# Optimization experiments

Hardware: AMD Instinct MI355X
Metric: run time of the kernel (lower is better)

Reference implementation:

```python
import jax, jax.numpy as jnp
import numpy as np

N_NODES = 50000
N_EDGES = 800000
HIDDEN = 128
NUM_LAYERS = 3
NEG_SLOPE = 0.2  # PyG GATConv default leaky_relu slope


def setup_inputs() -> dict:
    key = jax.random.key(0)
    ks = jax.random.split(key, 10)
    d = HIDDEN
    glorot = 1.0 / np.sqrt(d)
    inp = {
        "x": jax.random.normal(ks[0], (N_NODES, d), dtype=jnp.float32),
        "edge_index": jax.random.randint(ks[1], (2, N_EDGES), 0, N_NODES, dtype=jnp.int32),
        "edge_mask": jax.random.uniform(ks[2], (N_EDGES,), dtype=jnp.float32),
        # GATConv params (heads=1)
        "W_gat": jax.random.normal(ks[3], (d, d), dtype=jnp.float32) * glorot,
        "a_src": jax.random.normal(ks[4], (d,), dtype=jnp.float32) * glorot,
        "a_dst": jax.random.normal(ks[5], (d,), dtype=jnp.float32) * glorot,
        "b_gat": jnp.zeros((d,), dtype=jnp.float32),
        # Stacked GCNConv params
        "W_gcn": jax.random.normal(ks[6], (NUM_LAYERS, d, d), dtype=jnp.float32) * glorot,
        "b_gcn": jnp.zeros((NUM_LAYERS, d), dtype=jnp.float32),
    }
    return inp


def _seg_softmax(e, seg, n):
    m = jax.ops.segment_max(e, seg, num_segments=n)
    p = jnp.exp(e - m[seg])
    s = jax.ops.segment_sum(p, seg, num_segments=n)
    return p / s[seg]


def reference(x, edge_index, edge_mask, W_gat, a_src, a_dst, b_gat, W_gcn, b_gcn):
    N = x.shape[0]
    loops = jnp.arange(N, dtype=edge_index.dtype)
    src = jnp.concatenate([edge_index[0], loops])  # [E+N] with self loops
    dst = jnp.concatenate([edge_index[1], loops])

    # --- GATConv (heads=1, add_self_loops=True); edge_attr ignored (edge_dim=None) ---
    xp = x @ W_gat                                      # [N, d]
    e = jax.nn.leaky_relu((xp @ a_src)[src] + (xp @ a_dst)[dst], NEG_SLOPE)
    alpha = _seg_softmax(e, dst, N)                     # segment softmax over incoming edges
    h = jax.ops.segment_sum(alpha[:, None] * xp[src], dst, num_segments=N) + b_gat

    # --- GCN normalization with edge_mask as edge_weight (self-loop weight = 1) ---
    w = jnp.concatenate([edge_mask, jnp.ones((N,), dtype=edge_mask.dtype)])
    deg = jax.ops.segment_sum(w, dst, num_segments=N)
    dinv = jnp.where(deg > 0, jax.lax.rsqrt(jnp.maximum(deg, 1e-12)), 0.0)
    norm = dinv[src] * w * dinv[dst]                    # [E+N]

    outs = [h]
    for l in range(NUM_LAYERS):
        z = outs[-1] @ W_gcn[l]                         # [N, d]
        z = jax.ops.segment_sum(norm[:, None] * z[src], dst, num_segments=N) + b_gcn[l]
        outs.append(jax.nn.relu(z))

    # JumpingKnowledge 'max': elementwise max over layer outputs
    return jnp.max(jnp.stack(outs, axis=0), axis=0)
```

## Files before the change

### kernel.cpp

```cpp
#include <hip/hip_runtime.h>

#define HIDDEN 128
#define NEG_SLOPE 0.2f
#define P_SORT 256

typedef unsigned short ushort_t;
typedef __attribute__((ext_vector_type(8))) short short8;
typedef __attribute__((ext_vector_type(4))) float floatx4;

static inline size_t align_up(size_t x, size_t a){ return (x + a - 1) & ~(a - 1); }

__device__ __forceinline__ ushort_t f2b(float f){
  unsigned u = __float_as_uint(f);
  unsigned r = (u + 0x7FFFu + ((u >> 16) & 1u)) >> 16;
  return (ushort_t)r;
}

__device__ __forceinline__ void fma8(float* acc, uint4 v, float a){
  acc[0] += a * __uint_as_float(v.x << 16);
  acc[1] += a * __uint_as_float(v.x & 0xFFFF0000u);
  acc[2] += a * __uint_as_float(v.y << 16);
  acc[3] += a * __uint_as_float(v.y & 0xFFFF0000u);
  acc[4] += a * __uint_as_float(v.z << 16);
  acc[5] += a * __uint_as_float(v.z & 0xFFFF0000u);
  acc[6] += a * __uint_as_float(v.w << 16);
  acc[7] += a * __uint_as_float(v.w & 0xFFFF0000u);
}

__device__ __forceinline__ uint4 pack8(const float* f){
  uint4 u;
  u.x = (unsigned)f2b(f[0]) | ((unsigned)f2b(f[1]) << 16);
  u.y = (unsigned)f2b(f[2]) | ((unsigned)f2b(f[3]) << 16);
  u.z = (unsigned)f2b(f[4]) | ((unsigned)f2b(f[5]) << 16);
  u.w = (unsigned)f2b(f[6]) | ((unsigned)f2b(f[7]) << 16);
  return u;
}


__global__ __launch_bounds__(256) void k_b1cnt(const int* __restrict__ dst,
                                               int* __restrict__ bcnt,
                                               int E, int epb, int nbkt){
  __shared__ unsigned c[256];
  int t = threadIdx.x;
  c[t] = 0;
  __syncthreads();
  int e0 = blockIdx.x * epb;
  int e1 = min(E, e0 + epb);
  for (int e = e0 + t; e < e1; e += 256) atomicAdd(&c[dst[e] >> 8], 1u);
  __syncthreads();
  if (t < nbkt) bcnt[t * P_SORT + blockIdx.x] = (int)c[t];
}

__global__ void k_scan1(const int* __restrict__ in, int* __restrict__ incl,
                        int* __restrict__ blockSums, int M){
  __shared__ int sd[256];
  int t = threadIdx.x;
  int i = blockIdx.x*256 + t;
  int v = (i < M) ? in[i] : 0;
  sd[t] = v; __syncthreads();
  for (int off = 1; off < 256; off <<= 1){
    int add = (t >= off) ? sd[t-off] : 0;
    __syncthreads();
    sd[t] += add;
    __syncthreads();
  }
  if (i < M) incl[i] = sd[t];
  if (t == 255) blockSums[blockIdx.x] = sd[255];
}

__global__ void k_scan2(const int* __restrict__ blockSums, int* __restrict__ blockOffs, int nb){
  __shared__ int sd[256];
  __shared__ int carry;
  int t = threadIdx.x;
  if (t == 0) carry = 0;
  __syncthreads();
  for (int base = 0; base < nb; base += 256){
    int i = base + t;
    int v = (i < nb) ? blockSums[i] : 0;
    sd[t] = v; __syncthreads();
    for (int off = 1; off < 256; off <<= 1){
      int add = (t >= off) ? sd[t-off] : 0;
      __syncthreads();
      sd[t] += add;
      __syncthreads();
    }
    if (i < nb) blockOffs[i] = carry + sd[t] - v;
    __syncthreads();
    if (t == 0) carry += sd[255];
    __syncthreads();
  }
}

__global__ void k_scanex(int* __restrict__ arr, const int* __restrict__ in,
                         const int* __restrict__ blockOffs, int M){
  int i = blockIdx.x*256 + threadIdx.x;
  if (i < M) arr[i] = arr[i] - in[i] + blockOffs[blockIdx.x];
}

__global__ __launch_bounds__(256) void k_b1place(const int* __restrict__ src,
                                                 const int* __restrict__ dst,
                                                 const float* __restrict__ w,
                                                 const int* __restrict__ ebase,
                                                 unsigned* __restrict__ tpk,
                                                 float* __restrict__ tw,
                                                 int E, int epb){
  __shared__ unsigned c[256];
  int t = threadIdx.x;
  c[t] = 0;
  __syncthreads();
  int e0 = blockIdx.x * epb;
  int e1 = min(E, e0 + epb);
  for (int e = e0 + t; e < e1; e += 256){
    int d = dst[e];
    int b = d >> 8;
    unsigned r = atomicAdd(&c[b], 1u);
    int pos = ebase[b * P_SORT + blockIdx.x] + (int)r;
    tpk[pos] = (unsigned)src[e] | ((unsigned)(d & 255) << 16);
    tw[pos]  = w[e];
  }
}

__global__ __launch_bounds__(256) void k_b2(const unsigned* __restrict__ tpk,
                                            const float* __restrict__ tw,
                                            const int* __restrict__ ebase,
                                            int* __restrict__ col_src,
                                            float* __restrict__ col_w,
                                            int* __restrict__ rowp,
                                            float* __restrict__ dinv,
                                            int N, int E, int nbkt){
  __shared__ unsigned hcnt[256];
  __shared__ int sd[256];
  __shared__ int lofs[256];
  __shared__ unsigned rcnt[256];
  __shared__ float wsum[256];
  int b = blockIdx.x, t = threadIdx.x;
  int e0 = ebase[b * P_SORT];
  int e1 = (b + 1 < nbkt) ? ebase[(b + 1) * P_SORT] : E;
  hcnt[t] = 0; rcnt[t] = 0; wsum[t] = 0.f;
  __syncthreads();
  for (int e = e0 + t; e < e1; e += 256) atomicAdd(&hcnt[(tpk[e] >> 16) & 255u], 1u);
  __syncthreads();
  int v = (int)hcnt[t];
  sd[t] = v; __syncthreads();
  for (int off = 1; off < 256; off <<= 1){
    int add = (t >= off) ? sd[t-off] : 0;
    __syncthreads();
    sd[t] += add;
    __syncthreads();
  }
  lofs[t] = sd[t] - v;
  int node = b*256 + t;
  if (node < N) rowp[node] = e0 + sd[t] - v;
  if (b == 0 && t == 0) rowp[N] = E;
  __syncthreads();
  for (int e = e0 + t; e < e1; e += 256){
    unsigned pk = tpk[e];
    float wv = tw[e];
    unsigned dl = (pk >> 16) & 255u;
    unsigned r = atomicAdd(&rcnt[dl], 1u);
    int pos = e0 + lofs[dl] + (int)r;
    col_src[pos] = (int)(pk & 0xFFFFu);
    col_w[pos]   = wv;
    atomicAdd(&wsum[dl], wv);
  }
  __syncthreads();
  if (node < N) dinv[node] = rsqrtf(wsum[t] + 1.0f);
}

__global__ void k_edges(const int* __restrict__ rowp, const int* __restrict__ col_src,
                        const float* __restrict__ col_w, const float* __restrict__ dinv,
                        const float* __restrict__ ssrc, const float* __restrict__ sdst,
                        float* __restrict__ col_norm, float* __restrict__ col_e, int N){
  int n = blockIdx.x*16 + (threadIdx.x >> 4);
  int l = threadIdx.x & 15;
  if (n >= N) return;
  int rs = rowp[n], re = rowp[n+1];
  float dn = dinv[n], sd = sdst[n];
  for (int j = rs + l; j < re; j += 16){
    int s = col_src[j];
    col_norm[j] = dinv[s] * col_w[j] * dn;
    float ee = ssrc[s] + sd;
    col_e[j] = (ee >= 0.f) ? ee : NEG_SLOPE*ee;
  }
}


__global__ void k_cast_x(const float* __restrict__ x, unsigned* __restrict__ xb, long n2){
  long i = (long)blockIdx.x*256 + threadIdx.x;
  if (i >= n2) return;
  float2 v = ((const float2*)x)[i];
  xb[i] = (unsigned)f2b(v.x) | ((unsigned)f2b(v.y) << 16);
}

__global__ void k_cast_w(const float* __restrict__ Wg, const float* __restrict__ Wc,
                         ushort_t* __restrict__ Wt){
  int i = blockIdx.x*256 + threadIdx.x;
  int mat = i >> 14, idx = i & 16383;
  int k = idx >> 7, n = idx & 127;
  float v = (mat == 0) ? Wg[idx] : Wc[(mat-1)*16384 + idx];
  Wt[mat*16384 + n*128 + k] = f2b(v);
}

__global__ __launch_bounds__(256) void k_gemm(const ushort_t* __restrict__ A,
                                              const ushort_t* __restrict__ Wt,
                                              ushort_t* __restrict__ C, int M){
  int wave = threadIdx.x >> 6, l = threadIdx.x & 63;
  int q = l >> 4, lm = l & 15;
  int rowBase = blockIdx.x*128 + wave*32;
  floatx4 acc[2][8];
  #pragma unroll
  for (int mt = 0; mt < 2; mt++)
    #pragma unroll
    for (int nt = 0; nt < 8; nt++) acc[mt][nt] = (floatx4){0.f,0.f,0.f,0.f};

  #pragma unroll
  for (int kc = 0; kc < 4; kc++){
    int k0 = kc*32 + q*8;
    short8 a[2];
    #pragma unroll
    for (int mt = 0; mt < 2; mt++){
      long r = rowBase + mt*16 + lm;
      if (r < M) a[mt] = *(const short8*)(A + r*128 + k0);
      else       a[mt] = (short8){0,0,0,0,0,0,0,0};
    }
    #pragma unroll
    for (int nt = 0; nt < 8; nt++){
      short8 b = *(const short8*)(Wt + (nt*16 + lm)*128 + k0);
      acc[0][nt] = __builtin_amdgcn_mfma_f32_16x16x32_bf16(a[0], b, acc[0][nt], 0, 0, 0);
      acc[1][nt] = __builtin_amdgcn_mfma_f32_16x16x32_bf16(a[1], b, acc[1][nt], 0, 0, 0);
    }
  }
  #pragma unroll
  for (int mt = 0; mt < 2; mt++){
    #pragma unroll
    for (int r = 0; r < 4; r++){
      long row = rowBase + mt*16 + q*4 + r;
      if (row < M){
        #pragma unroll
        for (int nt = 0; nt < 8; nt++)
          C[row*128 + nt*16 + lm] = f2b(acc[mt][nt][r]);
      }
    }
  }
}

__global__ void k_sdots(const unsigned* __restrict__ xb, const float* __restrict__ a_src,
                        const float* __restrict__ a_dst, float* __restrict__ ssrc,
                        float* __restrict__ sdst, int N){
  int n = blockIdx.x*4 + (threadIdx.x >> 6);
  int lane = threadIdx.x & 63;
  if (n >= N) return;
  unsigned w = xb[(size_t)n*64 + lane];
  float v0 = __uint_as_float(w << 16);
  float v1 = __uint_as_float(w & 0xFFFF0000u);
  float2 as = ((const float2*)a_src)[lane];
  float2 ad = ((const float2*)a_dst)[lane];
  float ps = v0*as.x + v1*as.y;
  float pd = v0*ad.x + v1*ad.y;
  #pragma unroll
  for (int off = 32; off >= 1; off >>= 1){
    ps += __shfl_xor(ps, off, 64);
    pd += __shfl_xor(pd, off, 64);
  }
  if (lane == 0){ ssrc[n] = ps; sdst[n] = pd; }
}

__global__ void k_gat(const ushort_t* __restrict__ xb, const int* __restrict__ rowp,
                      const int* __restrict__ col_src, const float* __restrict__ col_e,
                      const float* __restrict__ ssrc, const float* __restrict__ sdst,
                      const float* __restrict__ b_gat, ushort_t* __restrict__ hb,
                      float* __restrict__ y, int N){
  int n = blockIdx.x*4 + (threadIdx.x >> 6);
  int l = threadIdx.x & 63;
  if (n >= N) return;
  int rs = rowp[n], re = rowp[n+1];
  float es = ssrc[n] + sdst[n];
  es = (es >= 0.f) ? es : NEG_SLOPE*es;
  float m = es;
  for (int j = rs + l; j < re; j += 64) m = fmaxf(m, col_e[j]);
  #pragma unroll
  for (int off = 32; off >= 1; off >>= 1) m = fmaxf(m, __shfl_xor(m, off, 64));
  float s = 0.f;
  for (int j = rs + l; j < re; j += 64) s += __expf(col_e[j] - m);
  #pragma unroll
  for (int off = 32; off >= 1; off >>= 1) s += __shfl_xor(s, off, 64);
  s += __expf(es - m);
  float inv = 1.f / s;
  float a0 = __expf(es - m) * inv;

  int sub = l >> 4, q = l & 15;
  const uint4* x16 = (const uint4*)xb;
  float acc[8] = {0.f,0.f,0.f,0.f,0.f,0.f,0.f,0.f};
  int deg = re - rs;
  int iters = (deg + 3) >> 2;
  for (int i = 0; i < iters; i++){
    int edge = rs + (i << 2) + sub;
    float a = 0.f; int sidx = n;
    if (edge < re){ sidx = col_src[edge]; a = __expf(col_e[edge] - m) * inv; }
    uint4 v = x16[(size_t)sidx*16 + q];
    fma8(acc, v, a);
  }
  #pragma unroll
  for (int j = 0; j < 8; j++){
    acc[j] += __shfl_xor(acc[j], 16, 64);
    acc[j] += __shfl_xor(acc[j], 32, 64);
  }
  if (sub == 0){
    uint4 v = x16[(size_t)n*16 + q];
    fma8(acc, v, a0);
    float4 b0 = ((const float4*)b_gat)[q*2];
    float4 b1 = ((const float4*)b_gat)[q*2 + 1];
    acc[0]+=b0.x; acc[1]+=b0.y; acc[2]+=b0.z; acc[3]+=b0.w;
    acc[4]+=b1.x; acc[5]+=b1.y; acc[6]+=b1.z; acc[7]+=b1.w;
    ((uint4*)hb)[(size_t)n*16 + q] = pack8(acc);
    float4* y4 = (float4*)y;
    y4[(size_t)n*32 + q*2]     = make_float4(acc[0], acc[1], acc[2], acc[3]);
    y4[(size_t)n*32 + q*2 + 1] = make_float4(acc[4], acc[5], acc[6], acc[7]);
  }
}

__global__ void k_gcn(const ushort_t* __restrict__ zb, const int* __restrict__ rowp,
                      const int* __restrict__ col_src, const float* __restrict__ col_norm,
                      const float* __restrict__ dinv, const float* __restrict__ bias,
                      ushort_t* __restrict__ hb, float* __restrict__ y, int N){
  int n = blockIdx.x*4 + (threadIdx.x >> 6);
  int l = threadIdx.x & 63;
  if (n >= N) return;
  int rs = rowp[n], re = rowp[n+1];
  float di = dinv[n];
  float sn = di * di;
  int sub = l >> 4, q = l & 15;
  const uint4* z16 = (const uint4*)zb;
  float acc[8] = {0.f,0.f,0.f,0.f,0.f,0.f,0.f,0.f};
  int deg = re - rs;
  int iters = (deg + 3) >> 2;
  for (int i = 0; i < iters; i++){
    int edge = rs + (i << 2) + sub;
    float a = 0.f; int sidx = n;
    if (edge < re){ sidx = col_src[edge]; a = col_norm[edge]; }
    uint4 v = z16[(size_t)sidx*16 + q];
    fma8(acc, v, a);
  }
  #pragma unroll
  for (int j = 0; j < 8; j++){
    acc[j] += __shfl_xor(acc[j], 16, 64);
    acc[j] += __shfl_xor(acc[j], 32, 64);
  }
  if (sub == 0){
    uint4 v = z16[(size_t)n*16 + q];
    fma8(acc, v, sn);
    float4 b0 = ((const float4*)bias)[q*2];
    float4 b1 = ((const float4*)bias)[q*2 + 1];
    acc[0]=fmaxf(acc[0]+b0.x,0.f); acc[1]=fmaxf(acc[1]+b0.y,0.f);
    acc[2]=fmaxf(acc[2]+b0.z,0.f); acc[3]=fmaxf(acc[3]+b0.w,0.f);
    acc[4]=fmaxf(acc[4]+b1.x,0.f); acc[5]=fmaxf(acc[5]+b1.y,0.f);
    acc[6]=fmaxf(acc[6]+b1.z,0.f); acc[7]=fmaxf(acc[7]+b1.w,0.f);
    ((uint4*)hb)[(size_t)n*16 + q] = pack8(acc);
    float4* y4 = (float4*)y;
    float4 y0 = y4[(size_t)n*32 + q*2];
    float4 y1 = y4[(size_t)n*32 + q*2 + 1];
    y0.x=fmaxf(y0.x,acc[0]); y0.y=fmaxf(y0.y,acc[1]); y0.z=fmaxf(y0.z,acc[2]); y0.w=fmaxf(y0.w,acc[3]);
    y1.x=fmaxf(y1.x,acc[4]); y1.y=fmaxf(y1.y,acc[5]); y1.z=fmaxf(y1.z,acc[6]); y1.w=fmaxf(y1.w,acc[7]);
    y4[(size_t)n*32 + q*2]     = y0;
    y4[(size_t)n*32 + q*2 + 1] = y1;
  }
}

extern "C" void kernel_launch(void* const* d_in, const int* in_sizes, int n_in,
                              void* d_out, int out_size, void* d_ws, size_t ws_size,
                              hipStream_t stream){
  const float* x      = (const float*)d_in[0];
  const int*   eidx   = (const int*)d_in[1];
  const float* emask  = (const float*)d_in[2];
  const float* W_gat  = (const float*)d_in[3];
  const float* a_src  = (const float*)d_in[4];
  const float* a_dst  = (const float*)d_in[5];
  const float* b_gat  = (const float*)d_in[6];
  const float* W_gcn  = (const float*)d_in[7];
  const float* b_gcn  = (const float*)d_in[8];
  int N = in_sizes[0] / HIDDEN;
  int E = in_sizes[1] / 2;
  const int* src = eidx;
  const int* dst = eidx + E;

  char* p = (char*)d_ws;
  auto carve = [&](size_t bytes)->char*{ char* q = p; p += align_up(bytes, 512); return q; };
  ushort_t* xb   = (ushort_t*)carve((size_t)N*HIDDEN*2);
  ushort_t* zb   = (ushort_t*)carve((size_t)N*HIDDEN*2);
  ushort_t* hb   = (ushort_t*)carve((size_t)N*HIDDEN*2);
  ushort_t* Wt   = (ushort_t*)carve((size_t)4*HIDDEN*HIDDEN*2);
  float* ssrc    = (float*)carve((size_t)N*4);
  float* sdst    = (float*)carve((size_t)N*4);
  float* dinv    = (float*)carve((size_t)N*4);
  int*   rowp    = (int*)  carve((size_t)(N+1)*4);
  int*   col_src = (int*)  carve((size_t)E*4);
  float* col_w   = (float*)carve((size_t)E*4);
  float* col_norm= (float*)carve((size_t)E*4);
  float* col_e   = (float*)carve((size_t)E*4);
  unsigned* tpk  = (unsigned*)carve((size_t)E*4);
  float* tw      = (float*)carve((size_t)E*4);
  int nbkt = (N + 255) >> 8;
  int M    = nbkt * P_SORT;
  int*   bcnt  = (int*)carve((size_t)M*4);
  int*   ebase = (int*)carve((size_t)M*4);
  int nbs = (M + 255) / 256;
  int*   blockSums = (int*)carve((size_t)nbs*4);
  int*   blockOffs = (int*)carve((size_t)nbs*4);
  (void)ws_size; (void)n_in; (void)out_size;

  int epb = (E + P_SORT - 1) / P_SORT;
  int gb  = (N + 127) / 128;
  int nwb = (N + 3) / 4;
  int nqb = (N + 15) / 16;
  long n2 = (long)N*64;
  int cb  = (int)((n2 + 255) / 256);

  k_b1cnt  <<<P_SORT, 256, 0, stream>>>(dst, bcnt, E, epb, nbkt);
  k_scan1  <<<nbs, 256, 0, stream>>>(bcnt, ebase, blockSums, M);
  k_scan2  <<<1,   256, 0, stream>>>(blockSums, blockOffs, nbs);
  k_scanex <<<nbs, 256, 0, stream>>>(ebase, bcnt, blockOffs, M);
  k_b1place<<<P_SORT, 256, 0, stream>>>(src, dst, emask, ebase, tpk, tw, E, epb);
  k_b2     <<<nbkt, 256, 0, stream>>>(tpk, tw, ebase, col_src, col_w, rowp, dinv, N, E, nbkt);

  k_cast_x<<<cb, 256, 0, stream>>>(x, (unsigned*)xb, n2);
  k_cast_w<<<(4*HIDDEN*HIDDEN)/256, 256, 0, stream>>>(W_gat, W_gcn, Wt);

  k_gemm <<<gb, 256, 0, stream>>>(xb, Wt, zb, N);
  k_sdots<<<nwb,256, 0, stream>>>((const unsigned*)zb, a_src, a_dst, ssrc, sdst, N);
  k_edges<<<nqb,256, 0, stream>>>(rowp, col_src, col_w, dinv, ssrc, sdst, col_norm, col_e, N);

  k_gat  <<<nwb,256, 0, stream>>>(zb, rowp, col_src, col_e, ssrc, sdst,
                                  b_gat, hb, (float*)d_out, N);
  for (int l = 0; l < 3; l++){
    k_gemm<<<gb, 256, 0, stream>>>(hb, Wt + (size_t)(l+1)*HIDDEN*HIDDEN, zb, N);
    k_gcn <<<nwb,256, 0, stream>>>(zb, rowp, col_src, col_norm, dinv,
                                   b_gcn + (size_t)l*HIDDEN, hb, (float*)d_out, N);
  }
}
```

Before: 393.9 us.

## Split feature aggregation into column chunks and precompute softmax coefficients

Softmax normalization moves into a separate k_soft kernel that writes per-edge alpha in place of col_e, plus a per-node self coefficient. GAT and GCN aggregation are merged into one templated k_agg that splits the 128 features into 4 column chunks, each handled by its own block group. Each wave now walks 16 edges at a time with 4 lanes per row chunk. This gives four times as many waves and more edges in flight per wave, aimed at hiding gather latency. The cost is that col_src and coefficients are re-read once per chunk and there is an extra launch plus a pass over col_e.

```diff
diff --git a/kernel.cpp b/kernel.cpp
--- a/kernel.cpp
+++ b/kernel.cpp
@@ -184,6 +184,29 @@
   }
 }
 
+__global__ void k_soft(const int* __restrict__ rowp, float* __restrict__ col_e,
+                       const float* __restrict__ ssrc, const float* __restrict__ sdst,
+                       float* __restrict__ selfa, int N){
+  int n = blockIdx.x*4 + (threadIdx.x >> 6);
+  int l = threadIdx.x & 63;
+  if (n >= N) return;
+  int rs = rowp[n], re = rowp[n+1];
+  float es = ssrc[n] + sdst[n];
+  es = (es >= 0.f) ? es : NEG_SLOPE*es;
+  float m = es;
+  for (int j = rs + l; j < re; j += 64) m = fmaxf(m, col_e[j]);
+  #pragma unroll
+  for (int off = 32; off >= 1; off >>= 1) m = fmaxf(m, __shfl_xor(m, off, 64));
+  float s = 0.f;
+  for (int j = rs + l; j < re; j += 64) s += __expf(col_e[j] - m);
+  #pragma unroll
+  for (int off = 32; off >= 1; off >>= 1) s += __shfl_xor(s, off, 64);
+  s += __expf(es - m);
+  float inv = 1.f / s;
+  for (int j = rs + l; j < re; j += 64) col_e[j] = __expf(col_e[j] - m) * inv;
+  if (l == 0) selfa[n] = __expf(es - m) * inv;
+}
+
 
 __global__ void k_cast_x(const float* __restrict__ x, unsigned* __restrict__ xb, long n2){
   long i = (long)blockIdx.x*256 + threadIdx.x;
@@ -265,104 +288,64 @@
   if (lane == 0){ ssrc[n] = ps; sdst[n] = pd; }
 }
 
-__global__ void k_gat(const ushort_t* __restrict__ xb, const int* __restrict__ rowp,
-                      const int* __restrict__ col_src, const float* __restrict__ col_e,
-                      const float* __restrict__ ssrc, const float* __restrict__ sdst,
-                      const float* __restrict__ b_gat, ushort_t* __restrict__ hb,
-                      float* __restrict__ y, int N){
-  int n = blockIdx.x*4 + (threadIdx.x >> 6);
+template<int MODE>
+__global__ __launch_bounds__(256) void k_agg(const ushort_t* __restrict__ feat,
+                                             const int* __restrict__ rowp,
+                                             const int* __restrict__ col_src,
+                                             const float* __restrict__ coef,
+                                             const float* __restrict__ selfc,
+                                             const float* __restrict__ bias,
+                                             ushort_t* __restrict__ out,
+                                             float* __restrict__ y, int N, int nwb){
+  int c   = blockIdx.x / nwb;
+  int blk = blockIdx.x - c*nwb;
+  int n = blk*4 + (threadIdx.x >> 6);
+  if (n >= N) return;
   int l = threadIdx.x & 63;
-  if (n >= N) return;
+  int sub = l >> 2, q = l & 3;
   int rs = rowp[n], re = rowp[n+1];
-  float es = ssrc[n] + sdst[n];
-  es = (es >= 0.f) ? es : NEG_SLOPE*es;
-  float m = es;
-  for (int j = rs + l; j < re; j += 64) m = fmaxf(m, col_e[j]);
-  #pragma unroll
-  for (int off = 32; off >= 1; off >>= 1) m = fmaxf(m, __shfl_xor(m, off, 64));
-  float s = 0.f;
-  for (int j = rs + l; j < re; j += 64) s += __expf(col_e[j] - m);
-  #pragma unroll
-  for (int off = 32; off >= 1; off >>= 1) s += __shfl_xor(s, off, 64);
-  s += __expf(es - m);
-  float inv = 1.f / s;
-  float a0 = __expf(es - m) * inv;
-
-  int sub = l >> 4, q = l & 15;
-  const uint4* x16 = (const uint4*)xb;
+  const uint4* f16 = (const uint4*)feat;
   float acc[8] = {0.f,0.f,0.f,0.f,0.f,0.f,0.f,0.f};
-  int deg = re - rs;
-  int iters = (deg + 3) >> 2;
-  for (int i = 0; i < iters; i++){
-    int edge = rs + (i << 2) + sub;
+  for (int base = rs; base < re; base += 16){
+    int edge = base + sub;
     float a = 0.f; int sidx = n;
-    if (edge < re){ sidx = col_src[edge]; a = __expf(col_e[edge] - m) * inv; }
-    uint4 v = x16[(size_t)sidx*16 + q];
+    if (edge < re){ sidx = col_src[edge]; a = coef[edge]; }
+    uint4 v = f16[(size_t)sidx*16 + c*4 + q];
     fma8(acc, v, a);
   }
   #pragma unroll
   for (int j = 0; j < 8; j++){
+    acc[j] += __shfl_xor(acc[j], 4, 64);
+    acc[j] += __shfl_xor(acc[j], 8, 64);
     acc[j] += __shfl_xor(acc[j], 16, 64);
     acc[j] += __shfl_xor(acc[j], 32, 64);
   }
   if (sub == 0){
-    uint4 v = x16[(size_t)n*16 + q];
-    fma8(acc, v, a0);
-    float4 b0 = ((const float4*)b_gat)[q*2];
-    float4 b1 = ((const float4*)b_gat)[q*2 + 1];
+    float sc = selfc[n];
+    if (MODE == 1) sc = sc * sc;
+    uint4 v = f16[(size_t)n*16 + c*4 + q];
+    fma8(acc, v, sc);
+    float4 b0 = ((const float4*)bias)[c*8 + q*2];
+    float4 b1 = ((const float4*)bias)[c*8 + q*2 + 1];
     acc[0]+=b0.x; acc[1]+=b0.y; acc[2]+=b0.z; acc[3]+=b0.w;
     acc[4]+=b1.x; acc[5]+=b1.y; acc[6]+=b1.z; acc[7]+=b1.w;
-    ((uint4*)hb)[(size_t)n*16 + q] = pack8(acc);
+    if (MODE == 1){
+      #pragma unroll
+      for (int j = 0; j < 8; j++) acc[j] = fmaxf(acc[j], 0.f);
+    }
+    ((uint4*)out)[(size_t)n*16 + c*4 + q] = pack8(acc);
     float4* y4 = (float4*)y;
-    y4[(size_t)n*32 + q*2]     = make_float4(acc[0], acc[1], acc[2], acc[3]);
-    y4[(size_t)n*32 + q*2 + 1] = make_float4(acc[4], acc[5], acc[6], acc[7]);
-  }
-}
-
-__global__ void k_gcn(const ushort_t* __restrict__ zb, const int* __restrict__ rowp,
-                      const int* __restrict__ col_src, const float* __restrict__ col_norm,
-                      const float* __restrict__ dinv, const float* __restrict__ bias,
-                      ushort_t* __restrict__ hb, float* __restrict__ y, int N){
-  int n = blockIdx.x*4 + (threadIdx.x >> 6);
-  int l = threadIdx.x & 63;
-  if (n >= N) return;
-  int rs = rowp[n], re = rowp[n+1];
-  float di = dinv[n];
-  float sn = di * di;
-  int sub = l >> 4, q = l & 15;
-  const uint4* z16 = (const uint4*)zb;
-  float acc[8] = {0.f,0.f,0.f,0.f,0.f,0.f,0.f,0.f};
-  int deg = re - rs;
-  int iters = (deg + 3) >> 2;
-  for (int i = 0; i < iters; i++){
-    int edge = rs + (i << 2) + sub;
-    float a = 0.f; int sidx = n;
-    if (edge < re){ sidx = col_src[edge]; a = col_norm[edge]; }
-    uint4 v = z16[(size_t)sidx*16 + q];
-    fma8(acc, v, a);
-  }
-  #pragma unroll
-  for (int j = 0; j < 8; j++){
-    acc[j] += __shfl_xor(acc[j], 16, 64);
-    acc[j] += __shfl_xor(acc[j], 32, 64);
-  }
-  if (sub == 0){
-    uint4 v = z16[(size_t)n*16 + q];
-    fma8(acc, v, sn);
-    float4 b0 = ((const float4*)bias)[q*2];
-    float4 b1 = ((const float4*)bias)[q*2 + 1];
-    acc[0]=fmaxf(acc[0]+b0.x,0.f); acc[1]=fmaxf(acc[1]+b0.y,0.f);
-    acc[2]=fmaxf(acc[2]+b0.z,0.f); acc[3]=fmaxf(acc[3]+b0.w,0.f);
-    acc[4]=fmaxf(acc[4]+b1.x,0.f); acc[5]=fmaxf(acc[5]+b1.y,0.f);
-    acc[6]=fmaxf(acc[6]+b1.z,0.f); acc[7]=fmaxf(acc[7]+b1.w,0.f);
-    ((uint4*)hb)[(size_t)n*16 + q] = pack8(acc);
-    float4* y4 = (float4*)y;
-    float4 y0 = y4[(size_t)n*32 + q*2];
-    float4 y1 = y4[(size_t)n*32 + q*2 + 1];
-    y0.x=fmaxf(y0.x,acc[0]); y0.y=fmaxf(y0.y,acc[1]); y0.z=fmaxf(y0.z,acc[2]); y0.w=fmaxf(y0.w,acc[3]);
-    y1.x=fmaxf(y1.x,acc[4]); y1.y=fmaxf(y1.y,acc[5]); y1.z=fmaxf(y1.z,acc[6]); y1.w=fmaxf(y1.w,acc[7]);
-    y4[(size_t)n*32 + q*2]     = y0;
-    y4[(size_t)n*32 + q*2 + 1] = y1;
+    size_t yi = (size_t)n*32 + c*8 + q*2;
+    float4 n0 = make_float4(acc[0], acc[1], acc[2], acc[3]);
+    float4 n1 = make_float4(acc[4], acc[5], acc[6], acc[7]);
+    if (MODE == 0){
+      y4[yi] = n0; y4[yi+1] = n1;
+    } else {
+      float4 y0 = y4[yi], y1 = y4[yi+1];
+      y0.x=fmaxf(y0.x,n0.x); y0.y=fmaxf(y0.y,n0.y); y0.z=fmaxf(y0.z,n0.z); y0.w=fmaxf(y0.w,n0.w);
+      y1.x=fmaxf(y1.x,n1.x); y1.y=fmaxf(y1.y,n1.y); y1.z=fmaxf(y1.z,n1.z); y1.w=fmaxf(y1.w,n1.w);
+      y4[yi] = y0; y4[yi+1] = y1;
+    }
   }
 }
 
@@ -392,6 +375,7 @@
   float* ssrc    = (float*)carve((size_t)N*4);
   float* sdst    = (float*)carve((size_t)N*4);
   float* dinv    = (float*)carve((size_t)N*4);
+  float* selfa   = (float*)carve((size_t)N*4);
   int*   rowp    = (int*)  carve((size_t)(N+1)*4);
   int*   col_src = (int*)  carve((size_t)E*4);
   float* col_w   = (float*)carve((size_t)E*4);
@@ -428,12 +412,13 @@
   k_gemm <<<gb, 256, 0, stream>>>(xb, Wt, zb, N);
   k_sdots<<<nwb,256, 0, stream>>>((const unsigned*)zb, a_src, a_dst, ssrc, sdst, N);
   k_edges<<<nqb,256, 0, stream>>>(rowp, col_src, col_w, dinv, ssrc, sdst, col_norm, col_e, N);
-
-  k_gat  <<<nwb,256, 0, stream>>>(zb, rowp, col_src, col_e, ssrc, sdst,
-                                  b_gat, hb, (float*)d_out, N);
+  k_soft <<<nwb,256, 0, stream>>>(rowp, col_e, ssrc, sdst, selfa, N);
+
+  k_agg<0><<<4*nwb, 256, 0, stream>>>(zb, rowp, col_src, col_e, selfa,
+                                      b_gat, hb, (float*)d_out, N, nwb);
   for (int l = 0; l < 3; l++){
     k_gemm<<<gb, 256, 0, stream>>>(hb, Wt + (size_t)(l+1)*HIDDEN*HIDDEN, zb, N);
-    k_gcn <<<nwb,256, 0, stream>>>(zb, rowp, col_src, col_norm, dinv,
-                                   b_gcn + (size_t)l*HIDDEN, hb, (float*)d_out, N);
-  }
-}
+    k_agg<1><<<4*nwb, 256, 0, stream>>>(zb, rowp, col_src, col_norm, dinv,
+                                        b_gcn + (size_t)l*HIDDEN, hb, (float*)d_out, N, nwb);
+  }
+}
```

After: 577.9 us. 1.47x slower.
